# Kernel tuning notes

Measured on AMD Instinct MI355X. Metric: run time of the kernel, lower is better.

## Reference

```python
import jax, jax.numpy as jnp
import numpy as np

B, N, F = 32, 1024, 64          # batch, total nodes, local_cnn_dims
P, n, m, e = 8, 128, 256, 1024  # partitions, nodes/part, neighbors/part, edges/part
EF, T, H, W, G, R, L2 = 8, 16, 128, 8, 128, 256, 128


def leaky(z, s):
    return jnp.where(z >= 0, z, s * z)


def setup_inputs() -> dict:
    key = jax.random.key(0)
    ks = jax.random.split(key, 32)
    s = 0.05
    return {
        "x": jax.random.normal(ks[0], (B, N, F), jnp.float32),
        "t": jax.random.normal(ks[1], (B, T), jnp.float32),
        "ef": jax.random.normal(ks[2], (P, e, EF + 1), jnp.float32),
        "linc": jax.random.uniform(ks[3], (P, n, e), jnp.float32) / 32.0,
        "rinc": jax.random.uniform(ks[4], (P, e, m), jnp.float32) / 16.0,
        "cap": jax.random.normal(ks[5], (P, n), jnp.float32),
        "k1_w": jax.random.normal(ks[6], (P, H, EF), jnp.float32) * s,
        "k1_b": jax.random.normal(ks[7], (P, H), jnp.float32) * s,
        "k2_w": jax.random.normal(ks[8], (P, H, T), jnp.float32) * s,
        "k3_w": jax.random.normal(ks[9], (P, H, F), jnp.float32) * s,
        "k4_w": jax.random.normal(ks[10], (P, H, F), jnp.float32) * s,
        "k5_w": jax.random.normal(ks[11], (P, W, H), jnp.float32) * s,
        "k5_b": jax.random.normal(ks[12], (P, W), jnp.float32) * s,
        "gc_w": jax.random.normal(ks[13], (P, G, W * F), jnp.float32) * s,
        "gc_b": jax.random.normal(ks[14], (P, G), jnp.float32) * s,
        "r0_w": jax.random.normal(ks[15], (P, R, G * n), jnp.float32) * 0.005,
        "r1_w": jax.random.normal(ks[16], (P, R, T), jnp.float32) * s,
        "r1_b": jax.random.normal(ks[17], (P, R), jnp.float32) * s,
        "r2_w": jax.random.normal(ks[18], (P, R, n), jnp.float32) * s,
        "r3_w": jax.random.normal(ks[19], (P, n, R), jnp.float32) * s,
        "r3_b": jax.random.normal(ks[20], (P, n), jnp.float32) * s,
        "conv_w": jax.random.normal(ks[21], (L2, G, P), jnp.float32) * s,
        "conv_b": jax.random.normal(ks[22], (L2,), jnp.float32) * s,
        "nodes_idx": jax.random.randint(ks[23], (P, n), 0, N),
        "nbr_idx": jax.random.randint(ks[24], (P, m), 0, N),
    }


def reference(x, t, ef, linc, rinc, cap,
              k1_w, k1_b, k2_w, k3_w, k4_w, k5_w, k5_b, gc_w, gc_b,
              r0_w, r1_w, r1_b, r2_w, r3_w, r3_b, conv_w, conv_b,
              nodes_idx, nbr_idx):
    # gather node subsets per partition
    xg = x[:, nodes_idx]                                   # [B,P,n,F]
    xn = x[:, nbr_idx]                                     # [B,P,m,F]
    rx = jnp.einsum('pem,bpmf->bpef', rinc, xn)            # rinc @ x[nbrs]
    lx = jnp.einsum('pne,bpnf->bpef', linc, xg)            # linc^T @ x[nodes]
    # edge-conditioned kernel
    k = (jnp.einsum('phc,pec->peh', k1_w, ef[..., :-1]) + k1_b[:, None, :])[None]
    k = k + jnp.einsum('pht,bt->bph', k2_w, t)[:, :, None, :]
    k = k + jnp.einsum('phf,bpef->bpeh', k3_w, lx)
    k = k + jnp.einsum('phf,bpef->bpeh', k4_w, rx)
    kernel = jax.nn.relu(jnp.einsum('pwh,bpeh->bpew', k5_w, leaky(k, 0.02))
                         + k5_b[:, None, :])               # [B,P,e,W]
    # message passing: linc @ (kernel * rx) over edges
    y = jnp.einsum('pne,bpew,bpef->bpnwf', linc, kernel, rx)  # [B,P,n,W,F]
    y = y.reshape(B, P, n, W * F)
    y = jax.nn.relu(jnp.einsum('pgk,bpnk->bpng', gc_w, y) + gc_b[:, None, :])
    # readout weights per node
    h = (jnp.einsum('prk,bpk->bpr', r0_w, y.reshape(B, P, n * G))
         + jnp.einsum('prt,bt->bpr', r1_w, t) + r1_b[None]
         + jnp.einsum('prn,pn->pr', r2_w, cap)[None])
    w = jax.nn.relu(jnp.einsum('pnr,bpr->bpn', r3_w, leaky(h, 0.01)) + r3_b[None])
    res = jnp.einsum('bpn,bpng->bpg', w, y)                # [B,P,G]
    # conv1d with kernel_size=P collapses partition axis
    out = leaky(jnp.einsum('lgp,bpg->bl', conv_w, res) + conv_b, 0.02)
    return out  # [B, L2]
```

## Files before the change

kernel.cpp:

```cpp
#include <hip/hip_runtime.h>
#include <math.h>

#define B_ 32
#define N_ 1024
#define F_ 64
#define P_ 8
#define n_ 128
#define m_ 256
#define e_ 1024
#define EF_ 8
#define T_ 16
#define H_ 128
#define W_ 8
#define G_ 128
#define R_ 256
#define L2_ 128

typedef unsigned short u16;
typedef unsigned int u32;
typedef __attribute__((ext_vector_type(8))) short bf16x8;
typedef __attribute__((ext_vector_type(4))) float f32x4;

__device__ __forceinline__ float leakyf(float z, float s) { return z >= 0.f ? z : s * z; }

__device__ __forceinline__ u16 f2bf(float f) {
    u32 u = __float_as_uint(f);
    u += 0x7FFFu + ((u >> 16) & 1u);
    return (u16)(u >> 16);
}
__device__ __forceinline__ float bf2f(u16 h) { return __uint_as_float(((u32)h) << 16); }
__device__ __forceinline__ u32 pk(float a, float b) { return (u32)f2bf(a) | ((u32)f2bf(b) << 16); }

__device__ __forceinline__ int swz64(int r, int c) {
    return r * 64 + ((((c >> 2) ^ ((r >> 3) & 15)) << 2) | (c & 3));
}
__device__ __forceinline__ float4 ld64(const float* lds, int r, int c4) {
    return *reinterpret_cast<const float4*>(lds + r * 64 + ((c4 ^ ((r >> 3) & 15)) << 2));
}

__device__ __forceinline__ int swzi(int row, int col) {
    return row * 64 + ((((col >> 3) ^ (row & 7)) << 3) | (col & 7));
}
__device__ __forceinline__ bf16x8 ldfrag(const u16* lds, int row, int kb) {
    return *reinterpret_cast<const bf16x8*>(lds + row * 64 + ((((kb >> 3) ^ (row & 7)) << 3)));
}
__device__ __forceinline__ int swzi128(int row, int col) {
    return row * 128 + ((((col >> 3) ^ (row & 7)) << 3) | (col & 7));
}
__device__ __forceinline__ bf16x8 ldfrag128(const u16* lds, int row, int kb) {
    return *reinterpret_cast<const bf16x8*>(lds + row * 128 + ((((kb >> 3) ^ (row & 7)) << 3)));
}

__global__ __launch_bounds__(256) void k_prep(const float* __restrict__ linc,
                                              const float* __restrict__ rinc,
                                              const float* __restrict__ gcw,
                                              u16* __restrict__ lincbf,
                                              u16* __restrict__ rincbf,
                                              u16* __restrict__ gcwbf) {
    int i = blockIdx.x * 256 + threadIdx.x;
    const float* src;
    u16* dst;
    int base;
    if (i < 262144) { src = linc; dst = lincbf; base = 0; }
    else if (i < 786432) { src = rinc; dst = rincbf; base = 262144; }
    else { src = gcw; dst = gcwbf; base = 786432; }
    int j = i - base;
    float4 v = reinterpret_cast<const float4*>(src)[j];
    ushort4 o = make_ushort4(f2bf(v.x), f2bf(v.y), f2bf(v.z), f2bf(v.w));
    reinterpret_cast<ushort4*>(dst)[j] = o;
}

__global__ __launch_bounds__(256) void k_prep2(const float* __restrict__ linc,
                                               const float* __restrict__ k4w,
                                               const float* __restrict__ k1w,
                                               const float* __restrict__ k2w,
                                               const float* __restrict__ k1b,
                                               const float* __restrict__ ef,
                                               const float* __restrict__ k5w,
                                               u16* __restrict__ lincT,
                                               u16* __restrict__ Bw,
                                               u16* __restrict__ efb,
                                               u16* __restrict__ k5wb) {
    const int blk = blockIdx.x, t = threadIdx.x;
    if (blk < 64) {
        const int p = blk >> 3, et = blk & 7, e0 = et * 128;
        __shared__ u16 S[128 * 128];
        {
            const int nn = t >> 1, seg = (t & 1) * 64;
            const float4* src = reinterpret_cast<const float4*>(
                linc + (size_t)(p * n_ + nn) * e_ + e0 + seg);
#pragma unroll
            for (int q = 0; q < 16; q += 2) {
                float4 a = src[q], b2 = src[q + 1];
                uint4 o = make_uint4(pk(a.x, a.y), pk(a.z, a.w), pk(b2.x, b2.y), pk(b2.z, b2.w));
                int colbase = seg + q * 4;
                int ch = (colbase >> 3) ^ (nn & 7);
                *reinterpret_cast<uint4*>(S + nn * 128 + ch * 8) = o;
            }
        }
        __syncthreads();
        {
            const int e = t >> 1, ns = (t & 1) * 64;
            u16* dst = lincT + ((size_t)(p * e_) + e0 + e) * n_ + ns;
#pragma unroll
            for (int q = 0; q < 8; q++) {
                u16 v[8];
#pragma unroll
                for (int k = 0; k < 8; k++) v[k] = S[swzi128(ns + q * 8 + k, e)];
                uint4 o = make_uint4((u32)v[0] | ((u32)v[1] << 16), (u32)v[2] | ((u32)v[3] << 16),
                                     (u32)v[4] | ((u32)v[5] << 16), (u32)v[6] | ((u32)v[7] << 16));
                *reinterpret_cast<uint4*>(dst + q * 8) = o;
            }
        }
    } else if (blk < 68) {
        int flat = (blk - 64) * 256 + t;
        int p = flat >> 7, h = flat & 127;
        u16* dst = Bw + (size_t)flat * 128;
        const float4* s4 = reinterpret_cast<const float4*>(k4w + (size_t)(p * H_ + h) * F_);
#pragma unroll
        for (int q = 0; q < 16; q += 2) {
            float4 a = s4[q], b2 = s4[q + 1];
            *reinterpret_cast<uint4*>(dst + q * 4) =
                make_uint4(pk(a.x, a.y), pk(a.z, a.w), pk(b2.x, b2.y), pk(b2.z, b2.w));
        }
        {
            const float4* s1 = reinterpret_cast<const float4*>(k1w + (size_t)(p * H_ + h) * EF_);
            float4 a = s1[0], b2 = s1[1];
            *reinterpret_cast<uint4*>(dst + 64) =
                make_uint4(pk(a.x, a.y), pk(a.z, a.w), pk(b2.x, b2.y), pk(b2.z, b2.w));
        }
        {
            const float4* s2 = reinterpret_cast<const float4*>(k2w + (size_t)(p * H_ + h) * T_);
#pragma unroll
            for (int q = 0; q < 4; q += 2) {
                float4 a = s2[q], b2 = s2[q + 1];
                *reinterpret_cast<uint4*>(dst + 72 + q * 4) =
                    make_uint4(pk(a.x, a.y), pk(a.z, a.w), pk(b2.x, b2.y), pk(b2.z, b2.w));
            }
        }
        *reinterpret_cast<uint4*>(dst + 88) = make_uint4((u32)f2bf(k1b[p * H_ + h]), 0, 0, 0);
        *reinterpret_cast<uint4*>(dst + 96) = make_uint4(0, 0, 0, 0);
        *reinterpret_cast<uint4*>(dst + 104) = make_uint4(0, 0, 0, 0);
        *reinterpret_cast<uint4*>(dst + 112) = make_uint4(0, 0, 0, 0);
        *reinterpret_cast<uint4*>(dst + 120) = make_uint4(0, 0, 0, 0);
    } else if (blk < 100) {
        int flat = (blk - 68) * 256 + t;
        const float* s = ef + (size_t)flat * (EF_ + 1);
        float v0 = s[0], v1 = s[1], v2 = s[2], v3 = s[3], v4 = s[4], v5 = s[5], v6 = s[6], v7 = s[7];
        *reinterpret_cast<uint4*>(efb + (size_t)flat * 8) =
            make_uint4(pk(v0, v1), pk(v2, v3), pk(v4, v5), pk(v6, v7));
    } else {
        int p = blk - 100;
        int row = t >> 4, col8 = (t & 15) * 8;
        uint4 o = make_uint4(0, 0, 0, 0);
        if (row < 8) {
            const float4* s = reinterpret_cast<const float4*>(k5w + (size_t)(p * W_ + row) * H_ + col8);
            float4 a = s[0], b2 = s[1];
            o = make_uint4(pk(a.x, a.y), pk(a.z, a.w), pk(b2.x, b2.y), pk(b2.z, b2.w));
        }
        int ch = (col8 >> 3) ^ (row & 7);
        *reinterpret_cast<uint4*>(k5wb + (size_t)p * 2048 + row * 128 + ch * 8) = o;
    }
}

__global__ __launch_bounds__(256) void k_rx(const float* __restrict__ x,
                                            const u16* __restrict__ rincbf,
                                            const int* __restrict__ nbr,
                                            u16* __restrict__ rxbf) {
    const int et = blockIdx.x, p = blockIdx.y, b = blockIdx.z;
    const int t = threadIdx.x, lane = t & 63, wid = t >> 6;
    __shared__ __align__(16) u16 A_lds[128 * 64];
    __shared__ __align__(16) u16 BT_lds[64 * 64];
    f32x4 acc[2][4];
#pragma unroll
    for (int i = 0; i < 2; i++)
#pragma unroll
        for (int j = 0; j < 4; j++) acc[i][j] = 0.f;

    const int e0 = et * 128;
    for (int c = 0; c < 4; c++) {
        const int m0 = c * 64;
        __syncthreads();
        {
            int ee = t >> 1, seg = t & 1;
            const uint4* src = reinterpret_cast<const uint4*>(
                rincbf + ((size_t)(p * e_ + e0 + ee) * m_ + m0 + seg * 32));
#pragma unroll
            for (int q = 0; q < 4; q++) {
                uint4 v = src[q];
                int ch = (seg * 4 + q) ^ (ee & 7);
                *reinterpret_cast<uint4*>(A_lds + ee * 64 + ch * 8) = v;
            }
        }
        {
            int mm = t >> 2, fq = (t & 3) * 16;
            int row = nbr[p * m_ + m0 + mm];
            const float4* sx = reinterpret_cast<const float4*>(
                x + (size_t)(b * N_ + row) * F_ + fq);
#pragma unroll
            for (int q = 0; q < 4; q++) {
                float4 v = sx[q];
                int f0 = fq + q * 4;
                BT_lds[swzi(f0 + 0, mm)] = f2bf(v.x);
                BT_lds[swzi(f0 + 1, mm)] = f2bf(v.y);
                BT_lds[swzi(f0 + 2, mm)] = f2bf(v.z);
                BT_lds[swzi(f0 + 3, mm)] = f2bf(v.w);
            }
        }
        __syncthreads();
        const int wm0 = wid * 32, r15 = lane & 15, g4 = lane >> 4;
#pragma unroll
        for (int ks = 0; ks < 2; ks++) {
            int kb = ks * 32 + g4 * 8;
            bf16x8 af[2], bfr[4];
#pragma unroll
            for (int mf = 0; mf < 2; mf++) af[mf] = ldfrag(A_lds, wm0 + mf * 16 + r15, kb);
#pragma unroll
            for (int nf = 0; nf < 4; nf++) bfr[nf] = ldfrag(BT_lds, nf * 16 + r15, kb);
#pragma unroll
            for (int mf = 0; mf < 2; mf++)
#pragma unroll
                for (int nf = 0; nf < 4; nf++)
                    acc[mf][nf] = __builtin_amdgcn_mfma_f32_16x16x32_bf16(af[mf], bfr[nf], acc[mf][nf], 0, 0, 0);
        }
    }
    const int r15 = lane & 15, g4 = lane >> 4;
#pragma unroll
    for (int mf = 0; mf < 2; mf++)
#pragma unroll
        for (int nf = 0; nf < 4; nf++)
#pragma unroll
            for (int r = 0; r < 4; r++) {
                int erow = e0 + wid * 32 + mf * 16 + g4 * 4 + r;
                int f = nf * 16 + r15;
                rxbf[((size_t)(b * P_ + p) * e_ + erow) * F_ + f] = f2bf(acc[mf][nf][r]);
            }
}

__global__ __launch_bounds__(256) void k_u(const float* __restrict__ x,
                                           const float* __restrict__ k3w,
                                           const int* __restrict__ nodes,
                                           u16* __restrict__ uT) {
    const int p = blockIdx.x, b = blockIdx.y;
    const int t = threadIdx.x;
    const int th = t & 15;
    const int tn = t >> 4;
    __shared__ float xg[128 * 64];
    __shared__ float kw[128 * 64];
    for (int idx = t; idx < 8192; idx += 256) {
        int r = idx >> 6, f = idx & 63;
        int row = nodes[p * n_ + r];
        xg[swz64(r, f)] = x[(size_t)(b * N_ + row) * F_ + f];
        kw[swz64(r, f)] = k3w[(size_t)(p * H_ + r) * F_ + f];
    }
    __syncthreads();
    float acc[8][8];
#pragma unroll
    for (int i = 0; i < 8; i++)
#pragma unroll
        for (int j = 0; j < 8; j++) acc[i][j] = 0.f;
#pragma unroll 2
    for (int k4 = 0; k4 < 16; k4++) {
        float4 xv[8];
#pragma unroll
        for (int i = 0; i < 8; i++) xv[i] = ld64(xg, tn * 8 + i, k4);
#pragma unroll
        for (int j = 0; j < 8; j++) {
            float4 kv = ld64(kw, th * 8 + j, k4);
#pragma unroll
            for (int i = 0; i < 8; i++) {
                acc[i][j] += xv[i].x * kv.x + xv[i].y * kv.y + xv[i].z * kv.z + xv[i].w * kv.w;
            }
        }
    }
#pragma unroll
    for (int j = 0; j < 8; j++) {
        uint4 o = make_uint4(pk(acc[0][j], acc[1][j]), pk(acc[2][j], acc[3][j]),
                             pk(acc[4][j], acc[5][j]), pk(acc[6][j], acc[7][j]));
        *reinterpret_cast<uint4*>(uT + ((size_t)(b * P_ + p) * H_ + th * 8 + j) * n_ + tn * 8) = o;
    }
}

__global__ __launch_bounds__(256) void k_kern(const u16* __restrict__ lincT,
                                              const u16* __restrict__ uT,
                                              const u16* __restrict__ rxbf,
                                              const u16* __restrict__ Bw,
                                              const u16* __restrict__ efb,
                                              const float* __restrict__ tin,
                                              const u16* __restrict__ k5wb,
                                              const float* __restrict__ k5b,
                                              float* __restrict__ kern) {
    const int et = blockIdx.x, p = blockIdx.y, b = blockIdx.z;
    const int t = threadIdx.x, lane = t & 63, wid = t >> 6;
    const int r15 = lane & 15, g4 = lane >> 4;
    const int wm = (wid >> 1) * 64, wn = (wid & 1) * 64;
    __shared__ __align__(16) u16 S[128 * 128 + 16 * 128];
    u16* A_lds = S;
    u16* B_lds = S + 8192;
    u16* k5l = S + 16384;

    {
        uint4 v = reinterpret_cast<const uint4*>(k5wb + (size_t)p * 2048)[t];
        reinterpret_cast<uint4*>(k5l)[t] = v;
    }
    uint4 tinlo, tinhi;
    {
        const float4* s = reinterpret_cast<const float4*>(tin + b * T_);
        float4 a = s[0], b2 = s[1], c2 = s[2], d2 = s[3];
        tinlo = make_uint4(pk(a.x, a.y), pk(a.z, a.w), pk(b2.x, b2.y), pk(b2.z, b2.w));
        tinhi = make_uint4(pk(c2.x, c2.y), pk(c2.z, c2.w), pk(d2.x, d2.y), pk(d2.z, d2.w));
    }

    f32x4 acc[4][4];
#pragma unroll
    for (int i = 0; i < 4; i++)
#pragma unroll
        for (int j = 0; j < 4; j++) acc[i][j] = 0.f;

    const int e0 = et * 128;
    const size_t pb_e = (size_t)(b * P_ + p) * e_;
    const int row = t >> 1, half = t & 1;

    for (int c = 0; c < 4; c++) {
        __syncthreads();
        if (c < 2) {
            const uint4* src = reinterpret_cast<const uint4*>(
                lincT + ((size_t)(p * e_) + e0 + row) * n_ + c * 64 + half * 32);
#pragma unroll
            for (int q = 0; q < 4; q++) {
                uint4 v = src[q];
                int ch = (half * 4 + q) ^ (row & 7);
                *reinterpret_cast<uint4*>(A_lds + row * 64 + ch * 8) = v;
            }
        } else if (c == 2) {
            const uint4* src = reinterpret_cast<const uint4*>(
                rxbf + (pb_e + e0 + row) * F_ + half * 32);
#pragma unroll
            for (int q = 0; q < 4; q++) {
                uint4 v = src[q];
                int ch = (half * 4 + q) ^ (row & 7);
                *reinterpret_cast<uint4*>(A_lds + row * 64 + ch * 8) = v;
            }
        } else {
            uint4 w[4];
            if (half == 0) {
                w[0] = *reinterpret_cast<const uint4*>(efb + ((size_t)(p * e_) + e0 + row) * 8);
                w[1] = tinlo;
                w[2] = tinhi;
                w[3] = make_uint4(0x00003F80u, 0, 0, 0);
            } else {
                w[0] = w[1] = w[2] = w[3] = make_uint4(0, 0, 0, 0);
            }
#pragma unroll
            for (int q = 0; q < 4; q++) {
                int ch = (half * 4 + q) ^ (row & 7);
                *reinterpret_cast<uint4*>(A_lds + row * 64 + ch * 8) = w[q];
            }
        }
        {
            const uint4* src;
            if (c < 2)
                src = reinterpret_cast<const uint4*>(
                    uT + ((size_t)(b * P_ + p) * H_ + row) * n_ + c * 64 + half * 32);
            else
                src = reinterpret_cast<const uint4*>(
                    Bw + (size_t)(p * H_ + row) * 128 + (c - 2) * 64 + half * 32);
#pragma unroll
            for (int q = 0; q < 4; q++) {
                uint4 v = src[q];
                int ch = (half * 4 + q) ^ (row & 7);
                *reinterpret_cast<uint4*>(B_lds + row * 64 + ch * 8) = v;
            }
        }
        __syncthreads();
#pragma unroll
        for (int ks = 0; ks < 2; ks++) {
            int kb = ks * 32 + g4 * 8;
            bf16x8 af[4], bfr[4];
#pragma unroll
            for (int mf = 0; mf < 4; mf++) af[mf] = ldfrag(A_lds, wm + mf * 16 + r15, kb);
#pragma unroll
            for (int nf = 0; nf < 4; nf++) bfr[nf] = ldfrag(B_lds, wn + nf * 16 + r15, kb);
#pragma unroll
            for (int mf = 0; mf < 4; mf++)
#pragma unroll
                for (int nf = 0; nf < 4; nf++)
                    acc[mf][nf] = __builtin_amdgcn_mfma_f32_16x16x32_bf16(af[mf], bfr[nf], acc[mf][nf], 0, 0, 0);
        }
    }
    __syncthreads();
    u16* Kl = S;
#pragma unroll
    for (int mf = 0; mf < 4; mf++)
#pragma unroll
        for (int nf = 0; nf < 4; nf++)
#pragma unroll
            for (int r = 0; r < 4; r++) {
                int er = wm + mf * 16 + g4 * 4 + r;
                int hc = wn + nf * 16 + r15;
                Kl[swzi128(er, hc)] = f2bf(leakyf(acc[mf][nf][r], 0.02f));
            }
    __syncthreads();
    f32x4 acc2[2];
    acc2[0] = 0.f;
    acc2[1] = 0.f;
#pragma unroll
    for (int ks = 0; ks < 4; ks++) {
        int kb = ks * 32 + g4 * 8;
        bf16x8 bf5 = ldfrag128(k5l, r15, kb);
#pragma unroll
        for (int mf2 = 0; mf2 < 2; mf2++) {
            bf16x8 af = ldfrag128(Kl, wid * 32 + mf2 * 16 + r15, kb);
            acc2[mf2] = __builtin_amdgcn_mfma_f32_16x16x32_bf16(af, bf5, acc2[mf2], 0, 0, 0);
        }
    }
    if (r15 < 8) {
        float kb5 = k5b[p * W_ + r15];
#pragma unroll
        for (int mf2 = 0; mf2 < 2; mf2++)
#pragma unroll
            for (int r = 0; r < 4; r++) {
                int er = e0 + wid * 32 + mf2 * 16 + g4 * 4 + r;
                kern[(pb_e + er) * W_ + r15] = fmaxf(acc2[mf2][r] + kb5, 0.f);
            }
    }
}

__global__ __launch_bounds__(256) void k_q(const u16* __restrict__ rxbf,
                                           const float* __restrict__ kernb,
                                           const u16* __restrict__ gcwbf,
                                           u16* __restrict__ QTbf) {
    const int et = blockIdx.x, p = blockIdx.y, b = blockIdx.z;
    const int t = threadIdx.x, lane = t & 63, wid = t >> 6;
    __shared__ __align__(16) u16 A_lds[128 * 64];
    __shared__ __align__(16) u16 BT_lds[128 * 64];
    f32x4 acc[4][4];
#pragma unroll
    for (int i = 0; i < 4; i++)
#pragma unroll
        for (int j = 0; j < 4; j++) acc[i][j] = 0.f;

    const int e0 = et * 128;
    const size_t pb_e = (size_t)(b * P_ + p) * e_;
    const int wm = (wid >> 1) * 64, wn = (wid & 1) * 64;
    const int r15 = lane & 15, g4 = lane >> 4;

    for (int w = 0; w < 8; w++) {
        __syncthreads();
        {
            int ee = t >> 1, seg = t & 1;
            float ksc = kernb[(pb_e + e0 + ee) * W_ + w];
            const uint4* src = reinterpret_cast<const uint4*>(rxbf + (pb_e + e0 + ee) * F_ + seg * 32);
#pragma unroll
            for (int q = 0; q < 4; q++) {
                uint4 v = src[q];
                u32 vv[4] = {v.x, v.y, v.z, v.w};
                u32 ov[4];
#pragma unroll
                for (int q2 = 0; q2 < 4; q2++) {
                    float f0 = bf2f((u16)(vv[q2] & 0xFFFF)) * ksc;
                    float f1 = bf2f((u16)(vv[q2] >> 16)) * ksc;
                    ov[q2] = (u32)f2bf(f0) | ((u32)f2bf(f1) << 16);
                }
                int ch = (seg * 4 + q) ^ (ee & 7);
                *reinterpret_cast<uint4*>(A_lds + ee * 64 + ch * 8) =
                    make_uint4(ov[0], ov[1], ov[2], ov[3]);
            }
        }
        {
            int gg = t >> 1, seg = t & 1;
            const uint4* src = reinterpret_cast<const uint4*>(
                gcwbf + (size_t)(p * G_ + gg) * 512 + w * 64 + seg * 32);
#pragma unroll
            for (int q = 0; q < 4; q++) {
                uint4 v = src[q];
                int ch = (seg * 4 + q) ^ (gg & 7);
                *reinterpret_cast<uint4*>(BT_lds + gg * 64 + ch * 8) = v;
            }
        }
        __syncthreads();
#pragma unroll
        for (int ks = 0; ks < 2; ks++) {
            int kb = ks * 32 + g4 * 8;
            bf16x8 af[4], bfr[4];
#pragma unroll
            for (int mf = 0; mf < 4; mf++) af[mf] = ldfrag(A_lds, wm + mf * 16 + r15, kb);
#pragma unroll
            for (int nf = 0; nf < 4; nf++) bfr[nf] = ldfrag(BT_lds, wn + nf * 16 + r15, kb);
#pragma unroll
            for (int mf = 0; mf < 4; mf++)
#pragma unroll
                for (int nf = 0; nf < 4; nf++)
                    acc[mf][nf] = __builtin_amdgcn_mfma_f32_16x16x32_bf16(af[mf], bfr[nf], acc[mf][nf], 0, 0, 0);
        }
    }
#pragma unroll
    for (int mf = 0; mf < 4; mf++)
#pragma unroll
        for (int nf = 0; nf < 4; nf++) {
            int g = wn + nf * 16 + r15;
            int er = e0 + wm + mf * 16 + g4 * 4;
            ushort4 o = make_ushort4(f2bf(acc[mf][nf][0]), f2bf(acc[mf][nf][1]),
                                     f2bf(acc[mf][nf][2]), f2bf(acc[mf][nf][3]));
            *reinterpret_cast<ushort4*>(QTbf + ((size_t)(b * P_ + p) * G_ + g) * e_ + er) = o;
        }
}

__global__ __launch_bounds__(256) void k_y2(const u16* __restrict__ lincbf,
                                            const u16* __restrict__ QTbf,
                                            const float* __restrict__ gcb,
                                            float* __restrict__ y2) {
    const int p = blockIdx.x, b = blockIdx.y;
    const int t = threadIdx.x, lane = t & 63, wid = t >> 6;
    __shared__ __align__(16) u16 A_lds[128 * 64];
    __shared__ __align__(16) u16 BT_lds[128 * 64];
    f32x4 acc[4][4];
#pragma unroll
    for (int i = 0; i < 4; i++)
#pragma unroll
        for (int j = 0; j < 4; j++) acc[i][j] = 0.f;

    const size_t pb_g = (size_t)(b * P_ + p) * G_;
    const int wm = (wid >> 1) * 64, wn = (wid & 1) * 64;
    const int r15 = lane & 15, g4 = lane >> 4;

    for (int c = 0; c < 16; c++) {
        const int e0 = c * 64;
        __syncthreads();
        {
            int nn = t >> 1, seg = t & 1;
            const uint4* src = reinterpret_cast<const uint4*>(
                lincbf + (size_t)(p * n_ + nn) * e_ + e0 + seg * 32);
#pragma unroll
            for (int q = 0; q < 4; q++) {
                uint4 v = src[q];
                int ch = (seg * 4 + q) ^ (nn & 7);
                *reinterpret_cast<uint4*>(A_lds + nn * 64 + ch * 8) = v;
            }
        }
        {
            int gg = t >> 1, seg = t & 1;
            const uint4* src = reinterpret_cast<const uint4*>(
                QTbf + (pb_g + gg) * e_ + e0 + seg * 32);
#pragma unroll
            for (int q = 0; q < 4; q++) {
                uint4 v = src[q];
                int ch = (seg * 4 + q) ^ (gg & 7);
                *reinterpret_cast<uint4*>(BT_lds + gg * 64 + ch * 8) = v;
            }
        }
        __syncthreads();
#pragma unroll
        for (int ks = 0; ks < 2; ks++) {
            int kb = ks * 32 + g4 * 8;
            bf16x8 af[4], bfr[4];
#pragma unroll
            for (int mf = 0; mf < 4; mf++) af[mf] = ldfrag(A_lds, wm + mf * 16 + r15, kb);
#pragma unroll
            for (int nf = 0; nf < 4; nf++) bfr[nf] = ldfrag(BT_lds, wn + nf * 16 + r15, kb);
#pragma unroll
            for (int mf = 0; mf < 4; mf++)
#pragma unroll
                for (int nf = 0; nf < 4; nf++)
                    acc[mf][nf] = __builtin_amdgcn_mfma_f32_16x16x32_bf16(af[mf], bfr[nf], acc[mf][nf], 0, 0, 0);
        }
    }
#pragma unroll
    for (int mf = 0; mf < 4; mf++)
#pragma unroll
        for (int nf = 0; nf < 4; nf++) {
            int g = wn + nf * 16 + r15;
            float gb = gcb[p * G_ + g];
#pragma unroll
            for (int r = 0; r < 4; r++) {
                int nrow = wm + mf * 16 + g4 * 4 + r;
                y2[((size_t)(b * P_ + p) * n_ + nrow) * G_ + g] = fmaxf(acc[mf][nf][r] + gb, 0.f);
            }
        }
}

__global__ __launch_bounds__(256) void k_h1(const float* __restrict__ r0w,
                                            const float* __restrict__ y2,
                                            float* __restrict__ hpart) {
    const int ks = blockIdx.x;
    const int rt = blockIdx.y;
    const int p  = blockIdx.z;
    const int t = threadIdx.x, lane = t & 63, wid = t >> 6;
    const int r15 = lane & 15, g4 = lane >> 4;
    __shared__ __align__(16) u16 A_lds[64 * 128];
    __shared__ __align__(16) u16 B_lds[32 * 128];
    const int kc = ks * 512;
    const int row0 = rt * 64;

    f32x4 acc[2];
    acc[0] = 0.f;
    acc[1] = 0.f;

    const int sar = t >> 2, sas = t & 3;
    const int sbb = t >> 3, sbs = t & 7;

    for (int it = 0; it < 4; it++) {
        __syncthreads();
        {
            const float4* src = reinterpret_cast<const float4*>(
                r0w + ((size_t)(p * R_) + row0 + sar) * 16384 + kc + it * 128 + sas * 32);
#pragma unroll
            for (int q = 0; q < 4; q++) {
                float4 a = src[q * 2], b2 = src[q * 2 + 1];
                uint4 o = make_uint4(pk(a.x, a.y), pk(a.z, a.w), pk(b2.x, b2.y), pk(b2.z, b2.w));
                int ch = (sas * 4 + q) ^ (sar & 7);
                *reinterpret_cast<uint4*>(A_lds + sar * 128 + ch * 8) = o;
            }
        }
        {
            const float4* src = reinterpret_cast<const float4*>(
                y2 + (size_t)(sbb * P_ + p) * 16384 + kc + it * 128 + sbs * 16);
            float4 a = src[0], b2 = src[1], c2 = src[2], d2 = src[3];
            uint4 o0 = make_uint4(pk(a.x, a.y), pk(a.z, a.w), pk(b2.x, b2.y), pk(b2.z, b2.w));
            uint4 o1 = make_uint4(pk(c2.x, c2.y), pk(c2.z, c2.w), pk(d2.x, d2.y), pk(d2.z, d2.w));
            int ch0 = (sbs * 2) ^ (sbb & 7);
            int ch1 = (sbs * 2 + 1) ^ (sbb & 7);
            *reinterpret_cast<uint4*>(B_lds + sbb * 128 + ch0 * 8) = o0;
            *reinterpret_cast<uint4*>(B_lds + sbb * 128 + ch1 * 8) = o1;
        }
        __syncthreads();
#pragma unroll
        for (int ksl = 0; ksl < 4; ksl++) {
            int kb = ksl * 32 + g4 * 8;
            bf16x8 af = ldfrag128(A_lds, wid * 16 + r15, kb);
#pragma unroll
            for (int nf = 0; nf < 2; nf++) {
                bf16x8 bfr = ldfrag128(B_lds, nf * 16 + r15, kb);
                acc[nf] = __builtin_amdgcn_mfma_f32_16x16x32_bf16(af, bfr, acc[nf], 0, 0, 0);
            }
        }
    }
#pragma unroll
    for (int nf = 0; nf < 2; nf++) {
        int b = nf * 16 + r15;
        int r = row0 + wid * 16 + g4 * 4;
        float4 v = make_float4(acc[nf][0], acc[nf][1], acc[nf][2], acc[nf][3]);
        *reinterpret_cast<float4*>(hpart + (((size_t)(ks * P_ + p) * 32 + b) * 256 + r)) = v;
    }
}

__global__ __launch_bounds__(128) void k_wres(const float* __restrict__ hpart,
                                              const float* __restrict__ r1w,
                                              const float* __restrict__ r1b,
                                              const float* __restrict__ r2w,
                                              const float* __restrict__ cap,
                                              const float* __restrict__ tin,
                                              const float* __restrict__ r3w,
                                              const float* __restrict__ r3b,
                                              const float* __restrict__ y2,
                                              float* __restrict__ res) {
    const int p = blockIdx.x, b = blockIdx.y;
    const int t = threadIdx.x;
    __shared__ float lh[256];
    __shared__ float wl[128];
    for (int rr = t; rr < 256; rr += 128) {
        float s = 0.f;
        for (int ks = 0; ks < 32; ks++)
            s += hpart[(((size_t)(ks * P_ + p) * 32 + b) * 256) + rr];
        for (int tt = 0; tt < T_; tt++) s += r1w[(size_t)(p * R_ + rr) * T_ + tt] * tin[b * T_ + tt];
        s += r1b[p * R_ + rr];
        for (int nn = 0; nn < n_; nn++) s += r2w[(size_t)(p * R_ + rr) * n_ + nn] * cap[p * n_ + nn];
        lh[rr] = leakyf(s, 0.01f);
    }
    __syncthreads();
    {
        const int nn = t;
        float accw = r3b[p * n_ + nn];
        const float* r3p = r3w + (size_t)(p * n_ + nn) * R_;
        for (int r = 0; r < 256; r += 4) {
            float4 rv = *reinterpret_cast<const float4*>(r3p + r);
            accw += rv.x * lh[r] + rv.y * lh[r + 1] + rv.z * lh[r + 2] + rv.w * lh[r + 3];
        }
        wl[nn] = fmaxf(accw, 0.f);
    }
    __syncthreads();
    {
        const int g = t;
        float a = 0.f;
        for (int nn = 0; nn < n_; nn++) a += wl[nn] * y2[((size_t)(b * P_ + p) * n_ + nn) * G_ + g];
        res[(b * P_ + p) * G_ + g] = a;
    }
}

__global__ __launch_bounds__(128) void k_out(const float* __restrict__ convw,
                                             const float* __restrict__ convb,
                                             const float* __restrict__ res,
                                             float* __restrict__ out) {
    const int b = blockIdx.x;
    const int t = threadIdx.x;
    __shared__ float rl[1024];
    for (int idx = t; idx < 1024; idx += 128) rl[idx] = res[b * 1024 + idx];
    __syncthreads();
    float a = convb[t];
    const float* cw = convw + (size_t)t * 1024;
    for (int gp = 0; gp < 1024; gp += 4) {
        float4 v = *reinterpret_cast<const float4*>(cw + gp);
        a += v.x * rl[((gp + 0) & 7) * 128 + ((gp + 0) >> 3)];
        a += v.y * rl[((gp + 1) & 7) * 128 + ((gp + 1) >> 3)];
        a += v.z * rl[((gp + 2) & 7) * 128 + ((gp + 2) >> 3)];
        a += v.w * rl[((gp + 3) & 7) * 128 + ((gp + 3) >> 3)];
    }
    out[b * L2_ + t] = leakyf(a, 0.02f);
}

extern "C" void kernel_launch(void* const* d_in, const int* in_sizes, int n_in,
                              void* d_out, int out_size, void* d_ws, size_t ws_size,
                              hipStream_t stream) {
    const float* x    = (const float*)d_in[0];
    const float* tin  = (const float*)d_in[1];
    const float* ef   = (const float*)d_in[2];
    const float* linc = (const float*)d_in[3];
    const float* rinc = (const float*)d_in[4];
    const float* cap  = (const float*)d_in[5];
    const float* k1w  = (const float*)d_in[6];
    const float* k1b  = (const float*)d_in[7];
    const float* k2w  = (const float*)d_in[8];
    const float* k3w  = (const float*)d_in[9];
    const float* k4w  = (const float*)d_in[10];
    const float* k5w  = (const float*)d_in[11];
    const float* k5b  = (const float*)d_in[12];
    const float* gcw  = (const float*)d_in[13];
    const float* gcb  = (const float*)d_in[14];
    const float* r0w  = (const float*)d_in[15];
    const float* r1w  = (const float*)d_in[16];
    const float* r1b  = (const float*)d_in[17];
    const float* r2w  = (const float*)d_in[18];
    const float* r3w  = (const float*)d_in[19];
    const float* r3b  = (const float*)d_in[20];
    const float* convw = (const float*)d_in[21];
    const float* convb = (const float*)d_in[22];
    const int* nodes  = (const int*)d_in[23];
    const int* nbr    = (const int*)d_in[24];
    float* out = (float*)d_out;

    float* ws = (float*)d_ws;
    u16*   rxbf   = (u16*)ws;
    u16*   uTbf   = (u16*)(ws + 8388608);
    float* kernb  = ws + 10485760;
    u16*   QTbf   = (u16*)(ws + 12582912);
    float* y2b    = ws + 29360128;
    u16*   lincbf = (u16*)(ws + 33554432);
    u16*   lincT  = (u16*)(ws + 34078720);
    u16*   rincbf = (u16*)(ws + 34603008);
    u16*   gcwbf  = (u16*)(ws + 35651584);
    u16*   Bwbf   = (u16*)(ws + 35913728);
    u16*   efbf   = (u16*)(ws + 35979264);
    u16*   k5wbf  = (u16*)(ws + 36012032);
    float* hpart  = ws;
    float* resb   = ws + 10485760;

    k_prep <<<3584, 256, 0, stream>>>(linc, rinc, gcw, lincbf, rincbf, gcwbf);
    k_prep2<<<108, 256, 0, stream>>>(linc, k4w, k1w, k2w, k1b, ef, k5w, lincT, Bwbf, efbf, k5wbf);
    k_rx  <<<dim3(8, P_, B_), 256, 0, stream>>>(x, rincbf, nbr, rxbf);
    k_u   <<<dim3(P_, B_),    256, 0, stream>>>(x, k3w, nodes, uTbf);
    k_kern<<<dim3(8, P_, B_), 256, 0, stream>>>(lincT, uTbf, rxbf, Bwbf, efbf, tin, k5wbf, k5b, kernb);
    k_q   <<<dim3(8, P_, B_), 256, 0, stream>>>(rxbf, kernb, gcwbf, QTbf);
    k_y2  <<<dim3(P_, B_),    256, 0, stream>>>(lincbf, QTbf, gcb, y2b);
    k_h1  <<<dim3(32, 4, P_), 256, 0, stream>>>(r0w, y2b, hpart);
    k_wres<<<dim3(P_, B_),    128, 0, stream>>>(hpart, r1w, r1b, r2w, cap, tin, r3w, r3b, y2b, resb);
    k_out <<<B_, 128, 0, stream>>>(convw, convb, resb, out);
}
```

Before: 268.4 us.

## Hoist rx tile out of w-loop and apply kernel scale post-MFMA

The k_q kernel now loads the rx tile and its A fragments into registers once, instead of rescaling and rewriting rx into LDS for each of the 8 kernel channels. The per-edge kernel scale is applied in fp32 to each MFMA partial result, and the gc weight slices are double-buffered in LDS so the next slice loads while the current one computes. This removes repeated global rx loads, bf16 convert work and one barrier per iteration. The cost is extra VALU multiply-adds, more registers for the held fragments, and slightly different rounding because the scaling no longer happens before bf16 quantisation.

```diff
diff --git a/kernel.cpp b/kernel.cpp
--- a/kernel.cpp
+++ b/kernel.cpp
@@ -432,67 +432,82 @@
                                            u16* __restrict__ QTbf) {
     const int et = blockIdx.x, p = blockIdx.y, b = blockIdx.z;
     const int t = threadIdx.x, lane = t & 63, wid = t >> 6;
-    __shared__ __align__(16) u16 A_lds[128 * 64];
-    __shared__ __align__(16) u16 BT_lds[128 * 64];
-    f32x4 acc[4][4];
-#pragma unroll
-    for (int i = 0; i < 4; i++)
-#pragma unroll
-        for (int j = 0; j < 4; j++) acc[i][j] = 0.f;
+    const int r15 = lane & 15, g4 = lane >> 4;
+    const int wm = (wid >> 1) * 64, wn = (wid & 1) * 64;
+    __shared__ __align__(16) u16 RX[128 * 64];
+    __shared__ __align__(16) u16 GW[2][128 * 64];
+    __shared__ float KL[8 * 128];
 
     const int e0 = et * 128;
     const size_t pb_e = (size_t)(b * P_ + p) * e_;
-    const int wm = (wid >> 1) * 64, wn = (wid & 1) * 64;
-    const int r15 = lane & 15, g4 = lane >> 4;
-
+    const int ee = t >> 1, seg = t & 1;
+
+    {
+        const uint4* src = reinterpret_cast<const uint4*>(rxbf + (pb_e + e0 + ee) * F_ + seg * 32);
+#pragma unroll
+        for (int q = 0; q < 4; q++) {
+            uint4 v = src[q];
+            int ch = (seg * 4 + q) ^ (ee & 7);
+            *reinterpret_cast<uint4*>(RX + ee * 64 + ch * 8) = v;
+        }
+        float4 kv = *reinterpret_cast<const float4*>(kernb + (pb_e + e0 + ee) * W_ + seg * 4);
+        KL[(seg * 4 + 0) * 128 + ee] = kv.x;
+        KL[(seg * 4 + 1) * 128 + ee] = kv.y;
+        KL[(seg * 4 + 2) * 128 + ee] = kv.z;
+        KL[(seg * 4 + 3) * 128 + ee] = kv.w;
+        const uint4* gsrc = reinterpret_cast<const uint4*>(
+            gcwbf + (size_t)(p * G_ + ee) * 512 + seg * 32);
+#pragma unroll
+        for (int q = 0; q < 4; q++) {
+            uint4 v = gsrc[q];
+            int ch = (seg * 4 + q) ^ (ee & 7);
+            *reinterpret_cast<uint4*>(GW[0] + ee * 64 + ch * 8) = v;
+        }
+    }
+    __syncthreads();
+
+    f32x4 acc[4][4];
+#pragma unroll
+    for (int i = 0; i < 4; i++)
+#pragma unroll
+        for (int j = 0; j < 4; j++) acc[i][j] = 0.f;
+
+    bf16x8 af[4][2];
+#pragma unroll
+    for (int mf = 0; mf < 4; mf++)
+#pragma unroll
+        for (int ks = 0; ks < 2; ks++)
+            af[mf][ks] = ldfrag(RX, wm + mf * 16 + r15, ks * 32 + g4 * 8);
+
+    const f32x4 zero = 0.f;
     for (int w = 0; w < 8; w++) {
-        __syncthreads();
-        {
-            int ee = t >> 1, seg = t & 1;
-            float ksc = kernb[(pb_e + e0 + ee) * W_ + w];
-            const uint4* src = reinterpret_cast<const uint4*>(rxbf + (pb_e + e0 + ee) * F_ + seg * 32);
-#pragma unroll
-            for (int q = 0; q < 4; q++) {
-                uint4 v = src[q];
-                u32 vv[4] = {v.x, v.y, v.z, v.w};
-                u32 ov[4];
-#pragma unroll
-                for (int q2 = 0; q2 < 4; q2++) {
-                    float f0 = bf2f((u16)(vv[q2] & 0xFFFF)) * ksc;
-                    float f1 = bf2f((u16)(vv[q2] >> 16)) * ksc;
-                    ov[q2] = (u32)f2bf(f0) | ((u32)f2bf(f1) << 16);
-                }
+        const int cur = w & 1;
+        if (w < 7) {
+            const uint4* gsrc = reinterpret_cast<const uint4*>(
+                gcwbf + (size_t)(p * G_ + ee) * 512 + (w + 1) * 64 + seg * 32);
+#pragma unroll
+            for (int q = 0; q < 4; q++) {
+                uint4 v = gsrc[q];
                 int ch = (seg * 4 + q) ^ (ee & 7);
-                *reinterpret_cast<uint4*>(A_lds + ee * 64 + ch * 8) =
-                    make_uint4(ov[0], ov[1], ov[2], ov[3]);
-            }
-        }
-        {
-            int gg = t >> 1, seg = t & 1;
-            const uint4* src = reinterpret_cast<const uint4*>(
-                gcwbf + (size_t)(p * G_ + gg) * 512 + w * 64 + seg * 32);
-#pragma unroll
-            for (int q = 0; q < 4; q++) {
-                uint4 v = src[q];
-                int ch = (seg * 4 + q) ^ (gg & 7);
-                *reinterpret_cast<uint4*>(BT_lds + gg * 64 + ch * 8) = v;
-            }
-        }
-        __syncthreads();
-#pragma unroll
-        for (int ks = 0; ks < 2; ks++) {
-            int kb = ks * 32 + g4 * 8;
-            bf16x8 af[4], bfr[4];
-#pragma unroll
-            for (int mf = 0; mf < 4; mf++) af[mf] = ldfrag(A_lds, wm + mf * 16 + r15, kb);
-#pragma unroll
-            for (int nf = 0; nf < 4; nf++) bfr[nf] = ldfrag(BT_lds, wn + nf * 16 + r15, kb);
-#pragma unroll
-            for (int mf = 0; mf < 4; mf++)
-#pragma unroll
-                for (int nf = 0; nf < 4; nf++)
-                    acc[mf][nf] = __builtin_amdgcn_mfma_f32_16x16x32_bf16(af[mf], bfr[nf], acc[mf][nf], 0, 0, 0);
-        }
+                *reinterpret_cast<uint4*>(GW[cur ^ 1] + ee * 64 + ch * 8) = v;
+            }
+        }
+        f32x4 kk[4];
+#pragma unroll
+        for (int mf = 0; mf < 4; mf++)
+            kk[mf] = *reinterpret_cast<const f32x4*>(KL + w * 128 + wm + mf * 16 + g4 * 4);
+#pragma unroll
+        for (int nf = 0; nf < 4; nf++) {
+            bf16x8 b0 = ldfrag(GW[cur], wn + nf * 16 + r15, g4 * 8);
+            bf16x8 b1 = ldfrag(GW[cur], wn + nf * 16 + r15, 32 + g4 * 8);
+#pragma unroll
+            for (int mf = 0; mf < 4; mf++) {
+                f32x4 macc = __builtin_amdgcn_mfma_f32_16x16x32_bf16(af[mf][0], b0, zero, 0, 0, 0);
+                macc = __builtin_amdgcn_mfma_f32_16x16x32_bf16(af[mf][1], b1, macc, 0, 0, 0);
+                acc[mf][nf] += kk[mf] * macc;
+            }
+        }
+        __syncthreads();
     }
 #pragma unroll
     for (int mf = 0; mf < 4; mf++)
```

After: 278.5 us. 3.8% more time.
